# Optimization experiments

Measured on AMD Instinct MI355X. Metric: run time of the kernel, lower is better.

The kernel has to match this reference:

```python
import jax, jax.numpy as jnp
import numpy as np

D_IN = 1024
D_OUT = 1024
NUM_HEADS = 16
HEAD_DIM = D_OUT // NUM_HEADS


def setup_inputs() -> dict:
    key = jax.random.key(0)
    ks = jax.random.split(key, 6)
    B, T = 2, 2048
    x = jax.random.normal(ks[0], (B, T, D_IN), dtype=jnp.float32)
    s = 1.0 / np.sqrt(D_IN)
    Wq = jax.random.normal(ks[1], (D_IN, D_OUT), dtype=jnp.float32) * s
    Wk = jax.random.normal(ks[2], (D_IN, D_OUT), dtype=jnp.float32) * s
    Wv = jax.random.normal(ks[3], (D_IN, D_OUT), dtype=jnp.float32) * s
    Wo = jax.random.normal(ks[4], (D_OUT, D_OUT), dtype=jnp.float32) * (1.0 / np.sqrt(D_OUT))
    bo = jnp.zeros((D_OUT,), dtype=jnp.float32)
    return {"x": x, "Wq": Wq, "Wk": Wk, "Wv": Wv, "Wo": Wo, "bo": bo}


def reference(x, Wq, Wk, Wv, Wo, bo):
    B, T, _ = x.shape
    # project and split heads -> (B, H, T, Dh)
    def split(t):
        return t.reshape(B, T, NUM_HEADS, HEAD_DIM).transpose(0, 2, 1, 3)
    Q = split(x @ Wq)
    K = split(x @ Wk)
    V = split(x @ Wv)
    scale = HEAD_DIM ** -0.5
    scores = jnp.einsum('bhqd,bhkd->bhqk', Q, K) * scale  # (B,H,T,T)
    causal = jnp.triu(jnp.ones((T, T), dtype=bool), k=1)
    scores = jnp.where(causal, -jnp.inf, scores)
    weights = jax.nn.softmax(scores, axis=-1)
    ctx = jnp.einsum('bhqk,bhkd->bhqd', weights, V)  # (B,H,T,Dh)
    ctx = ctx.transpose(0, 2, 1, 3).reshape(B, T, D_OUT)
    return ctx @ Wo + bo
```

## Files before the change

### kernel.cpp

```cpp
#include <hip/hip_runtime.h>
#include <hip/hip_bf16.h>

#define NH   16
#define HD   64
#define BB   2
#define TT   2048
#define DIN  1024
#define DOUT 1024
#define MTOT (BB*TT)

#define QSCALE 0.18033688011112042f
#define MAXC   20.0f

typedef __hip_bfloat16 bf16;
typedef short bf16x8  __attribute__((ext_vector_type(8)));
typedef float f32x4   __attribute__((ext_vector_type(4)));
typedef float f32x16  __attribute__((ext_vector_type(16)));

__device__ __forceinline__ bf16 f2bf(float f){ return __float2bfloat16(f); }

__device__ __forceinline__ void gld16(const bf16* g, bf16* l){
    __builtin_amdgcn_global_load_lds(
        (const __attribute__((address_space(1))) unsigned int*)g,
        (__attribute__((address_space(3))) unsigned int*)l,
        16, 0, 0);
}

__device__ __forceinline__ size_t qk_off(int bh, int t, int d){
    return (size_t)bh*131072 + (size_t)(((t>>5)*4 + (d>>4))*512)
         + ((t&31) + 32*((d>>3)&1))*8 + (d&7);
}
__device__ __forceinline__ size_t v_off(int bh, int t, int d){
    return (size_t)bh*131072 + (size_t)((((t>>4)*2) + (d>>5))*512)
         + ((d&31) + 32*((t>>2)&1))*8 + ((t&3) + 4*((t>>3)&1));
}

__global__ void prep_all(const float* __restrict__ x,
                         const float* __restrict__ Wq, const float* __restrict__ Wk,
                         const float* __restrict__ Wv, const float* __restrict__ Wo,
                         bf16* __restrict__ xb, bf16* __restrict__ WT){
    __shared__ float tile[64][65];
    const int blk = blockIdx.x;
    if (blk < 4096){
        int i = blk*256 + threadIdx.x;
        float4 v = ((const float4*)x)[i];
        bf16 o[4] = {f2bf(v.x), f2bf(v.y), f2bf(v.z), f2bf(v.w)};
        *(ushort4*)&xb[(size_t)i*4] = *(ushort4*)o;
        return;
    }
    const int wb = blk - 4096;
    const int n0 = (wb >> 4) * 64, k0 = (wb & 15) * 64;
    const float* W;
    switch (n0 >> 10){ case 0: W=Wq; break; case 1: W=Wk; break; case 2: W=Wv; break; default: W=Wo; }
    const int c0 = n0 & 1023;
    const int tr = threadIdx.x >> 6;
    const int tc = threadIdx.x & 63;
    #pragma unroll
    for (int it = 0; it < 16; it++){
        int k = k0 + it*4 + tr;
        tile[it*4 + tr][tc] = W[(size_t)k*DOUT + c0 + tc];
    }
    __syncthreads();
    #pragma unroll
    for (int it = 0; it < 16; it++){
        int n = it*4 + tr;
        WT[(size_t)(n0 + n)*DIN + k0 + tc] = f2bf(tile[tc][n]);
    }
}

__launch_bounds__(256)
__global__ void gemm_qkv(const bf16* __restrict__ Xb, const bf16* __restrict__ WT,
                         bf16* __restrict__ Qf, bf16* __restrict__ Kf, bf16* __restrict__ Vf){
    __shared__ __align__(16) bf16 As[128*64];
    __shared__ __align__(16) bf16 Bs[128*64];
    const int n0 = blockIdx.x * 128;
    const int m0 = blockIdx.y * 128;
    const int tid = threadIdx.x;
    const int wave = tid >> 6, lane = tid & 63;
    const int wm = (wave & 1) * 64, wn = (wave >> 1) * 64;
    const int quad = lane >> 4, l16 = lane & 15;
    const int srow = wave*8 + (lane >> 3);
    const int schk = lane & 7;

    f32x4 acc[4][4] = {};
    for (int k0 = 0; k0 < DIN; k0 += 64){
        #pragma unroll
        for (int j = 0; j < 4; j++){
            int r = srow + j*32;
            int gc = (schk ^ (r & 7)) << 3;
            gld16(&Xb[(size_t)(m0 + r)*DIN + k0 + gc], &As[r*64 + schk*8]);
            gld16(&WT[(size_t)(n0 + r)*DIN + k0 + gc], &Bs[r*64 + schk*8]);
        }
        __syncthreads();
        #pragma unroll
        for (int ks = 0; ks < 2; ks++){
            bf16x8 af[4], bfr[4];
            #pragma unroll
            for (int mi = 0; mi < 4; mi++){
                int row = wm + mi*16 + l16;
                af[mi] = *(bf16x8*)&As[row*64 + (((ks*4 + quad) ^ (row & 7)) << 3)];
            }
            #pragma unroll
            for (int ni = 0; ni < 4; ni++){
                int row = wn + ni*16 + l16;
                bfr[ni] = *(bf16x8*)&Bs[row*64 + (((ks*4 + quad) ^ (row & 7)) << 3)];
            }
            #pragma unroll
            for (int mi = 0; mi < 4; mi++)
                #pragma unroll
                for (int ni = 0; ni < 4; ni++)
                    acc[mi][ni] = __builtin_amdgcn_mfma_f32_16x16x32_bf16(af[mi], bfr[ni], acc[mi][ni], 0, 0, 0);
        }
        __syncthreads();
    }
    #pragma unroll
    for (int mi = 0; mi < 4; mi++){
        #pragma unroll
        for (int ni = 0; ni < 4; ni++){
            int col = n0 + wn + ni*16 + l16;
            int which = col >> 10;
            int c = col & 1023;
            int h = c >> 6, d = c & 63;
            int m_base = m0 + wm + mi*16 + quad*4;
            int b = m_base >> 11, t0 = m_base & 2047;
            int bh = b*NH + h;
            if (which == 2){
                bf16 pk[4];
                #pragma unroll
                for (int r = 0; r < 4; r++) pk[r] = f2bf(acc[mi][ni][r]);
                *(ushort4*)&Vf[v_off(bh, t0, d)] = *(ushort4*)pk;
            } else if (which == 0){
                #pragma unroll
                for (int r = 0; r < 4; r++)
                    Qf[qk_off(bh, t0 + r, d)] = f2bf(acc[mi][ni][r] * QSCALE);
            } else {
                #pragma unroll
                for (int r = 0; r < 4; r++)
                    Kf[qk_off(bh, t0 + r, d)] = f2bf(acc[mi][ni][r]);
            }
        }
    }
}

__launch_bounds__(256, 4)
__global__ void attn(const bf16* __restrict__ Qf, const bf16* __restrict__ Kf,
                     const bf16* __restrict__ Vf, bf16* __restrict__ ctx){
    __shared__ float Lo[3*64*36];
    __shared__ float Ls[3*64];
    const int blk  = blockIdx.x;
    const int bh   = (blk & 7) + 8*((blk >> 3) & 3);
    const int qb   = 63 - (blk >> 5);
    const int wave = threadIdx.x >> 6, lane = threadIdx.x & 63;
    const int n    = qb + 1;
    const int tstart = (n*wave) >> 2;
    const int tend   = ((n*(wave+1)) >> 2) - 1;
    const int h32  = lane >> 5, l32 = lane & 31;
    const int b    = bh >> 4, head = bh & 15;
    const bf16* Qb = Qf + (size_t)bh*131072 + lane*8;
    const bf16* Kb = Kf + (size_t)bh*131072 + lane*8;
    const bf16* Vb = Vf + (size_t)bh*131072 + lane*8;

    bf16x8 qf[4];
    #pragma unroll
    for (int ks = 0; ks < 4; ks++)
        qf[ks] = *(const bf16x8*)(Qb + (qb*4 + ks)*512);

    bf16x8 kc[4], vc[4];
    #pragma unroll
    for (int i = 0; i < 4; i++){
        kc[i] = *(const bf16x8*)(Kb + (tstart*4 + i)*512);
        vc[i] = *(const bf16x8*)(Vb + (tstart*4 + i)*512);
    }

    f32x16 o0 = {}, o1 = {};
    float lsum = 0.f;

    for (int tb = tstart; tb <= tend; tb++){
        f32x16 s = {};
        #pragma unroll
        for (int ks = 0; ks < 4; ks++)
            s = __builtin_amdgcn_mfma_f32_32x32x16_bf16(kc[ks], qf[ks], s, 0, 0, 0);
        if (tb < tend){
            #pragma unroll
            for (int i = 0; i < 4; i++)
                kc[i] = *(const bf16x8*)(Kb + ((tb+1)*4 + i)*512);
        }
        if (tb == qb){
            #pragma unroll
            for (int r = 0; r < 16; r++){
                int trow = (r&3) + 8*(r>>2) + 4*h32;
                if (trow > l32) s[r] = -1e30f;
            }
        }
        float p[16];
        #pragma unroll
        for (int r = 0; r < 16; r++){
            p[r] = __builtin_amdgcn_exp2f(s[r] - MAXC);
            lsum += p[r];
        }
        #pragma unroll
        for (int ki = 0; ki < 2; ki++){
            bf16 pb[8];
            #pragma unroll
            for (int j = 0; j < 8; j++) pb[j] = f2bf(p[ki*8 + j]);
            bf16x8 pbv = *(bf16x8*)pb;
            o0 = __builtin_amdgcn_mfma_f32_32x32x16_bf16(vc[ki*2+0], pbv, o0, 0, 0, 0);
            o1 = __builtin_amdgcn_mfma_f32_32x32x16_bf16(vc[ki*2+1], pbv, o1, 0, 0, 0);
        }
        if (tb < tend){
            #pragma unroll
            for (int i = 0; i < 4; i++)
                vc[i] = *(const bf16x8*)(Vb + ((tb+1)*4 + i)*512);
        }
    }

    if (wave != 0){
        float* lo = &Lo[(wave-1)*2304 + lane*36];
        #pragma unroll
        for (int c = 0; c < 4; c++){
            f32x4 w4 = { o0[c*4+0], o0[c*4+1], o0[c*4+2], o0[c*4+3] };
            *(f32x4*)&lo[c*4] = w4;
        }
        #pragma unroll
        for (int c = 0; c < 4; c++){
            f32x4 w4 = { o1[c*4+0], o1[c*4+1], o1[c*4+2], o1[c*4+3] };
            *(f32x4*)&lo[16 + c*4] = w4;
        }
        Ls[(wave-1)*64 + lane] = lsum;
    }
    __syncthreads();
    if (wave == 0){
        float lc = lsum;
        #pragma unroll
        for (int w = 0; w < 3; w++){
            const float* lo = &Lo[w*2304 + lane*36];
            #pragma unroll
            for (int c = 0; c < 4; c++){
                f32x4 r4 = *(const f32x4*)&lo[c*4];
                #pragma unroll
                for (int i = 0; i < 4; i++) o0[c*4+i] += r4[i];
            }
            #pragma unroll
            for (int c = 0; c < 4; c++){
                f32x4 r4 = *(const f32x4*)&lo[16 + c*4];
                #pragma unroll
                for (int i = 0; i < 4; i++) o1[c*4+i] += r4[i];
            }
            lc += Ls[w*64 + lane];
        }
        float lq  = lc + __shfl_xor(lc, 32);
        float inv = 1.0f / lq;
        const int q = qb*32 + l32;
        bf16* cp = ctx + ((size_t)(b*TT + q))*DOUT + head*HD;
        #pragma unroll
        for (int db = 0; db < 2; db++){
            #pragma unroll
            for (int rq = 0; rq < 4; rq++){
                bf16 pk[4];
                #pragma unroll
                for (int i = 0; i < 4; i++){
                    float ov = (db ? o1[rq*4 + i] : o0[rq*4 + i]) * inv;
                    pk[i] = f2bf(ov);
                }
                int d0 = db*32 + rq*8 + h32*4;
                *(ushort4*)&cp[d0] = *(ushort4*)pk;
            }
        }
    }
}

__launch_bounds__(256)
__global__ void gemm_out(const bf16* __restrict__ Cx, const bf16* __restrict__ WoT,
                         const float* __restrict__ bo, float* __restrict__ out){
    __shared__ __align__(16) bf16 As[128*64];
    __shared__ __align__(16) bf16 Bs[64*64];
    const int n0 = blockIdx.x * 64;
    const int m0 = blockIdx.y * 128;
    const int tid = threadIdx.x;
    const int wave = tid >> 6, lane = tid & 63;
    const int wm = (wave & 1) * 64, wn = (wave >> 1) * 32;
    const int quad = lane >> 4, l16 = lane & 15;
    const int srow = wave*8 + (lane >> 3);
    const int schk = lane & 7;

    f32x4 acc[4][2] = {};
    for (int k0 = 0; k0 < DOUT; k0 += 64){
        #pragma unroll
        for (int j = 0; j < 4; j++){
            int r = srow + j*32;
            int gc = (schk ^ (r & 7)) << 3;
            gld16(&Cx[(size_t)(m0 + r)*DOUT + k0 + gc], &As[r*64 + schk*8]);
        }
        #pragma unroll
        for (int j = 0; j < 2; j++){
            int r = srow + j*32;
            int gc = (schk ^ (r & 7)) << 3;
            gld16(&WoT[(size_t)(n0 + r)*DOUT + k0 + gc], &Bs[r*64 + schk*8]);
        }
        __syncthreads();
        #pragma unroll
        for (int ks = 0; ks < 2; ks++){
            bf16x8 af[4], bfr[2];
            #pragma unroll
            for (int mi = 0; mi < 4; mi++){
                int row = wm + mi*16 + l16;
                af[mi] = *(bf16x8*)&As[row*64 + (((ks*4 + quad) ^ (row & 7)) << 3)];
            }
            #pragma unroll
            for (int ni = 0; ni < 2; ni++){
                int row = wn + ni*16 + l16;
                bfr[ni] = *(bf16x8*)&Bs[row*64 + (((ks*4 + quad) ^ (row & 7)) << 3)];
            }
            #pragma unroll
            for (int mi = 0; mi < 4; mi++)
                #pragma unroll
                for (int ni = 0; ni < 2; ni++)
                    acc[mi][ni] = __builtin_amdgcn_mfma_f32_16x16x32_bf16(af[mi], bfr[ni], acc[mi][ni], 0, 0, 0);
        }
        __syncthreads();
    }
    #pragma unroll
    for (int mi = 0; mi < 4; mi++){
        #pragma unroll
        for (int ni = 0; ni < 2; ni++){
            int nn = n0 + wn + ni*16 + l16;
            float bias = bo[nn];
            #pragma unroll
            for (int r = 0; r < 4; r++){
                int m = m0 + wm + mi*16 + quad*4 + r;
                out[(size_t)m*DOUT + nn] = acc[mi][ni][r] + bias;
            }
        }
    }
}

extern "C" void kernel_launch(void* const* d_in, const int* in_sizes, int n_in,
                              void* d_out, int out_size, void* d_ws, size_t ws_size,
                              hipStream_t stream){
    const float* x  = (const float*)d_in[0];
    const float* Wq = (const float*)d_in[1];
    const float* Wk = (const float*)d_in[2];
    const float* Wv = (const float*)d_in[3];
    const float* Wo = (const float*)d_in[4];
    const float* bo = (const float*)d_in[5];
    float* out = (float*)d_out;

    char* ws = (char*)d_ws;
    bf16* xb  = (bf16*)(ws);
    bf16* WT  = (bf16*)(ws + ((size_t)8  << 20));
    bf16* Qf  = (bf16*)(ws + ((size_t)16 << 20));
    bf16* Kf  = (bf16*)(ws + ((size_t)24 << 20));
    bf16* Vf  = (bf16*)(ws + ((size_t)32 << 20));
    bf16* ctx = (bf16*)(ws + ((size_t)40 << 20));
    bf16* WoT = WT + (size_t)3072*DIN;

    prep_all <<<dim3(5120),    256, 0, stream>>>(x, Wq, Wk, Wv, Wo, xb, WT);
    gemm_qkv <<<dim3(24, 32),  256, 0, stream>>>(xb, WT, Qf, Kf, Vf);
    attn     <<<dim3(2048),    256, 0, stream>>>(Qf, Kf, Vf, ctx);
    gemm_out <<<dim3(16, 32),  256, 0, stream>>>(ctx, WoT, bo, out);
}
```

Baseline: 172.8 us.

## Pre-swizzle GEMM operands into MFMA fragment layout and load directly to registers

The prep kernel and the attention epilogue now write X, the weights and the context in a fragment-tiled layout, so each lane's 8-element MFMA operand is one contiguous 16-byte load. Both projection GEMMs drop LDS staging and barriers and load fragments straight from global memory into double-buffered registers. Tile shapes change to 256x64 and 256x32 with 1D grids. This removes shared-memory traffic and synchronisation, but there is no operand sharing between waves, so each wave refetches the B tile from global/L2, which raises cache bandwidth pressure.

```diff
diff --git a/kernel.cpp b/kernel.cpp
--- a/kernel.cpp
+++ b/kernel.cpp
@@ -19,13 +19,9 @@
 
 __device__ __forceinline__ bf16 f2bf(float f){ return __float2bfloat16(f); }
 
-__device__ __forceinline__ void gld16(const bf16* g, bf16* l){
-    __builtin_amdgcn_global_load_lds(
-        (const __attribute__((address_space(1))) unsigned int*)g,
-        (__attribute__((address_space(3))) unsigned int*)l,
-        16, 0, 0);
-}
-
+__device__ __forceinline__ size_t frag_off(int r, int k){
+    return (size_t)((r>>4)*32 + (k>>5))*512 + (size_t)(((r&15) + 16*((k>>3)&3))*8) + (k&7);
+}
 __device__ __forceinline__ size_t qk_off(int bh, int t, int d){
     return (size_t)bh*131072 + (size_t)(((t>>5)*4 + (d>>4))*512)
          + ((t&31) + 32*((d>>3)&1))*8 + (d&7);
@@ -38,14 +34,15 @@
 __global__ void prep_all(const float* __restrict__ x,
                          const float* __restrict__ Wq, const float* __restrict__ Wk,
                          const float* __restrict__ Wv, const float* __restrict__ Wo,
-                         bf16* __restrict__ xb, bf16* __restrict__ WT){
+                         bf16* __restrict__ Xf, bf16* __restrict__ Wf){
     __shared__ float tile[64][65];
     const int blk = blockIdx.x;
     if (blk < 4096){
         int i = blk*256 + threadIdx.x;
         float4 v = ((const float4*)x)[i];
         bf16 o[4] = {f2bf(v.x), f2bf(v.y), f2bf(v.z), f2bf(v.w)};
-        *(ushort4*)&xb[(size_t)i*4] = *(ushort4*)o;
+        int m = i >> 8, k = (i & 255) << 2;
+        *(ushort4*)&Xf[frag_off(m, k)] = *(ushort4*)o;
         return;
     }
     const int wb = blk - 4096;
@@ -62,66 +59,64 @@
     }
     __syncthreads();
     #pragma unroll
-    for (int it = 0; it < 16; it++){
-        int n = it*4 + tr;
-        WT[(size_t)(n0 + n)*DIN + k0 + tc] = f2bf(tile[tc][n]);
-    }
-}
-
-__launch_bounds__(256)
-__global__ void gemm_qkv(const bf16* __restrict__ Xb, const bf16* __restrict__ WT,
+    for (int it = 0; it < 4; it++){
+        int n_loc = tc;
+        int k_loc = ((tr*4) + it) * 4;
+        bf16 o[4];
+        #pragma unroll
+        for (int j = 0; j < 4; j++) o[j] = f2bf(tile[k_loc + j][n_loc]);
+        *(ushort4*)&Wf[frag_off(n0 + n_loc, k0 + k_loc)] = *(ushort4*)o;
+    }
+}
+
+__launch_bounds__(256, 3)
+__global__ void gemm_qkv(const bf16* __restrict__ Xf, const bf16* __restrict__ Wf,
                          bf16* __restrict__ Qf, bf16* __restrict__ Kf, bf16* __restrict__ Vf){
-    __shared__ __align__(16) bf16 As[128*64];
-    __shared__ __align__(16) bf16 Bs[128*64];
-    const int n0 = blockIdx.x * 128;
-    const int m0 = blockIdx.y * 128;
-    const int tid = threadIdx.x;
-    const int wave = tid >> 6, lane = tid & 63;
-    const int wm = (wave & 1) * 64, wn = (wave >> 1) * 64;
+    const int blk = blockIdx.x;
+    const int n0 = (blk % 48) * 64;
+    const int m0 = (blk / 48) * 256;
+    const int wave = threadIdx.x >> 6, lane = threadIdx.x & 63;
     const int quad = lane >> 4, l16 = lane & 15;
-    const int srow = wave*8 + (lane >> 3);
-    const int schk = lane & 7;
-
+    const bf16* Ab = Xf + (size_t)((m0 >> 4) + wave*4)*32*512 + lane*8;
+    const bf16* Bb = Wf + (size_t)(n0 >> 4)*32*512 + lane*8;
+
+    bf16x8 af[2][4], bfr[2][4];
+    #pragma unroll
+    for (int s = 0; s < 2; s++){
+        #pragma unroll
+        for (int i = 0; i < 4; i++){
+            af[s][i]  = *(const bf16x8*)(Ab + ((size_t)i*32 + s)*512);
+            bfr[s][i] = *(const bf16x8*)(Bb + ((size_t)i*32 + s)*512);
+        }
+    }
     f32x4 acc[4][4] = {};
-    for (int k0 = 0; k0 < DIN; k0 += 64){
-        #pragma unroll
-        for (int j = 0; j < 4; j++){
-            int r = srow + j*32;
-            int gc = (schk ^ (r & 7)) << 3;
-            gld16(&Xb[(size_t)(m0 + r)*DIN + k0 + gc], &As[r*64 + schk*8]);
-            gld16(&WT[(size_t)(n0 + r)*DIN + k0 + gc], &Bs[r*64 + schk*8]);
-        }
-        __syncthreads();
-        #pragma unroll
-        for (int ks = 0; ks < 2; ks++){
-            bf16x8 af[4], bfr[4];
-            #pragma unroll
-            for (int mi = 0; mi < 4; mi++){
-                int row = wm + mi*16 + l16;
-                af[mi] = *(bf16x8*)&As[row*64 + (((ks*4 + quad) ^ (row & 7)) << 3)];
-            }
-            #pragma unroll
-            for (int ni = 0; ni < 4; ni++){
-                int row = wn + ni*16 + l16;
-                bfr[ni] = *(bf16x8*)&Bs[row*64 + (((ks*4 + quad) ^ (row & 7)) << 3)];
-            }
+    for (int kt = 0; kt < 32; kt += 2){
+        #pragma unroll
+        for (int s = 0; s < 2; s++){
             #pragma unroll
             for (int mi = 0; mi < 4; mi++)
                 #pragma unroll
                 for (int ni = 0; ni < 4; ni++)
-                    acc[mi][ni] = __builtin_amdgcn_mfma_f32_16x16x32_bf16(af[mi], bfr[ni], acc[mi][ni], 0, 0, 0);
-        }
-        __syncthreads();
+                    acc[mi][ni] = __builtin_amdgcn_mfma_f32_16x16x32_bf16(af[s][mi], bfr[s][ni], acc[mi][ni], 0, 0, 0);
+            int kn = kt + 2 + s;
+            if (kn < 32){
+                #pragma unroll
+                for (int i = 0; i < 4; i++){
+                    af[s][i]  = *(const bf16x8*)(Ab + ((size_t)i*32 + kn)*512);
+                    bfr[s][i] = *(const bf16x8*)(Bb + ((size_t)i*32 + kn)*512);
+                }
+            }
+        }
     }
     #pragma unroll
     for (int mi = 0; mi < 4; mi++){
         #pragma unroll
         for (int ni = 0; ni < 4; ni++){
-            int col = n0 + wn + ni*16 + l16;
+            int col = n0 + ni*16 + l16;
             int which = col >> 10;
             int c = col & 1023;
             int h = c >> 6, d = c & 63;
-            int m_base = m0 + wm + mi*16 + quad*4;
+            int m_base = m0 + wave*64 + mi*16 + quad*4;
             int b = m_base >> 11, t0 = m_base & 2047;
             int bh = b*NH + h;
             if (which == 2){
@@ -251,7 +246,7 @@
         float lq  = lc + __shfl_xor(lc, 32);
         float inv = 1.0f / lq;
         const int q = qb*32 + l32;
-        bf16* cp = ctx + ((size_t)(b*TT + q))*DOUT + head*HD;
+        const int mrow = b*TT + q;
         #pragma unroll
         for (int db = 0; db < 2; db++){
             #pragma unroll
@@ -262,72 +257,59 @@
                     float ov = (db ? o1[rq*4 + i] : o0[rq*4 + i]) * inv;
                     pk[i] = f2bf(ov);
                 }
-                int d0 = db*32 + rq*8 + h32*4;
-                *(ushort4*)&cp[d0] = *(ushort4*)pk;
-            }
-        }
-    }
-}
-
-__launch_bounds__(256)
-__global__ void gemm_out(const bf16* __restrict__ Cx, const bf16* __restrict__ WoT,
+                int ch = head*HD + db*32 + rq*8 + h32*4;
+                *(ushort4*)&ctx[frag_off(mrow, ch)] = *(ushort4*)pk;
+            }
+        }
+    }
+}
+
+__launch_bounds__(256, 2)
+__global__ void gemm_out(const bf16* __restrict__ Cf, const bf16* __restrict__ Wf,
                          const float* __restrict__ bo, float* __restrict__ out){
-    __shared__ __align__(16) bf16 As[128*64];
-    __shared__ __align__(16) bf16 Bs[64*64];
-    const int n0 = blockIdx.x * 64;
-    const int m0 = blockIdx.y * 128;
-    const int tid = threadIdx.x;
-    const int wave = tid >> 6, lane = tid & 63;
-    const int wm = (wave & 1) * 64, wn = (wave >> 1) * 32;
+    const int blk = blockIdx.x;
+    const int n0 = (blk % 32) * 32;
+    const int m0 = (blk / 32) * 256;
+    const int wave = threadIdx.x >> 6, lane = threadIdx.x & 63;
     const int quad = lane >> 4, l16 = lane & 15;
-    const int srow = wave*8 + (lane >> 3);
-    const int schk = lane & 7;
-
+    const bf16* Ab = Cf + (size_t)((m0 >> 4) + wave*4)*32*512 + lane*8;
+    const bf16* Bb = Wf + (size_t)((3072 + n0) >> 4)*32*512 + lane*8;
+
+    bf16x8 af[2][4], bfr[2][2];
+    #pragma unroll
+    for (int s = 0; s < 2; s++){
+        #pragma unroll
+        for (int i = 0; i < 4; i++) af[s][i]  = *(const bf16x8*)(Ab + ((size_t)i*32 + s)*512);
+        #pragma unroll
+        for (int i = 0; i < 2; i++) bfr[s][i] = *(const bf16x8*)(Bb + ((size_t)i*32 + s)*512);
+    }
     f32x4 acc[4][2] = {};
-    for (int k0 = 0; k0 < DOUT; k0 += 64){
-        #pragma unroll
-        for (int j = 0; j < 4; j++){
-            int r = srow + j*32;
-            int gc = (schk ^ (r & 7)) << 3;
-            gld16(&Cx[(size_t)(m0 + r)*DOUT + k0 + gc], &As[r*64 + schk*8]);
-        }
-        #pragma unroll
-        for (int j = 0; j < 2; j++){
-            int r = srow + j*32;
-            int gc = (schk ^ (r & 7)) << 3;
-            gld16(&WoT[(size_t)(n0 + r)*DOUT + k0 + gc], &Bs[r*64 + schk*8]);
-        }
-        __syncthreads();
-        #pragma unroll
-        for (int ks = 0; ks < 2; ks++){
-            bf16x8 af[4], bfr[2];
-            #pragma unroll
-            for (int mi = 0; mi < 4; mi++){
-                int row = wm + mi*16 + l16;
-                af[mi] = *(bf16x8*)&As[row*64 + (((ks*4 + quad) ^ (row & 7)) << 3)];
-            }
-            #pragma unroll
-            for (int ni = 0; ni < 2; ni++){
-                int row = wn + ni*16 + l16;
-                bfr[ni] = *(bf16x8*)&Bs[row*64 + (((ks*4 + quad) ^ (row & 7)) << 3)];
-            }
+    for (int kt = 0; kt < 32; kt += 2){
+        #pragma unroll
+        for (int s = 0; s < 2; s++){
             #pragma unroll
             for (int mi = 0; mi < 4; mi++)
                 #pragma unroll
                 for (int ni = 0; ni < 2; ni++)
-                    acc[mi][ni] = __builtin_amdgcn_mfma_f32_16x16x32_bf16(af[mi], bfr[ni], acc[mi][ni], 0, 0, 0);
-        }
-        __syncthreads();
+                    acc[mi][ni] = __builtin_amdgcn_mfma_f32_16x16x32_bf16(af[s][mi], bfr[s][ni], acc[mi][ni], 0, 0, 0);
+            int kn = kt + 2 + s;
+            if (kn < 32){
+                #pragma unroll
+                for (int i = 0; i < 4; i++) af[s][i]  = *(const bf16x8*)(Ab + ((size_t)i*32 + kn)*512);
+                #pragma unroll
+                for (int i = 0; i < 2; i++) bfr[s][i] = *(const bf16x8*)(Bb + ((size_t)i*32 + kn)*512);
+            }
+        }
     }
     #pragma unroll
     for (int mi = 0; mi < 4; mi++){
         #pragma unroll
         for (int ni = 0; ni < 2; ni++){
-            int nn = n0 + wn + ni*16 + l16;
+            int nn = n0 + ni*16 + l16;
             float bias = bo[nn];
             #pragma unroll
             for (int r = 0; r < 4; r++){
-                int m = m0 + wm + mi*16 + quad*4 + r;
+                int m = m0 + wave*64 + mi*16 + quad*4 + r;
                 out[(size_t)m*DOUT + nn] = acc[mi][ni][r] + bias;
             }
         }
@@ -346,16 +328,15 @@
     float* out = (float*)d_out;
 
     char* ws = (char*)d_ws;
-    bf16* xb  = (bf16*)(ws);
-    bf16* WT  = (bf16*)(ws + ((size_t)8  << 20));
+    bf16* Xf  = (bf16*)(ws);
+    bf16* Wf  = (bf16*)(ws + ((size_t)8  << 20));
     bf16* Qf  = (bf16*)(ws + ((size_t)16 << 20));
     bf16* Kf  = (bf16*)(ws + ((size_t)24 << 20));
     bf16* Vf  = (bf16*)(ws + ((size_t)32 << 20));
-    bf16* ctx = (bf16*)(ws + ((size_t)40 << 20));
-    bf16* WoT = WT + (size_t)3072*DIN;
-
-    prep_all <<<dim3(5120),    256, 0, stream>>>(x, Wq, Wk, Wv, Wo, xb, WT);
-    gemm_qkv <<<dim3(24, 32),  256, 0, stream>>>(xb, WT, Qf, Kf, Vf);
-    attn     <<<dim3(2048),    256, 0, stream>>>(Qf, Kf, Vf, ctx);
-    gemm_out <<<dim3(16, 32),  256, 0, stream>>>(ctx, WoT, bo, out);
-}
+    bf16* Cf  = (bf16*)(ws + ((size_t)40 << 20));
+
+    prep_all <<<dim3(5120), 256, 0, stream>>>(x, Wq, Wk, Wv, Wo, Xf, Wf);
+    gemm_qkv <<<dim3(768),  256, 0, stream>>>(Xf, Wf, Qf, Kf, Vf);
+    attn     <<<dim3(2048), 256, 0, stream>>>(Qf, Kf, Vf, Cf);
+    gemm_out <<<dim3(512),  256, 0, stream>>>(Cf, Wf, bo, out);
+}
```

After: 180.9 us. +4.7%, slower.
